# Kernel optimization log

Hardware: AMD Instinct MI355X
Metric: run time of the kernel (lower is better)

Reference implementation:

```python
import jax, jax.numpy as jnp
import numpy as np


def _conv1x1(x, W, b):
    # 1x1 conv == per-pixel channel matmul: x [B,C,H,W], W [O,C], b [O]
    return jnp.einsum('bchw,oc->bohw', x, W) + b[None, :, None, None]


def setup_inputs() -> dict:
    key = jax.random.key(0)
    ks = jax.random.split(key, 9)
    B, C, H, W = 16, 512, 32, 32
    s = 1.0 / np.sqrt(C)
    inp = {
        'x': jax.random.normal(ks[0], (B, C, H, W), dtype=jnp.float32),
        'Wq': jax.random.normal(ks[1], (C, C), dtype=jnp.float32) * s,
        'bq': jax.random.normal(ks[2], (C,), dtype=jnp.float32) * 0.01,
        'Wk': jax.random.normal(ks[3], (C, C), dtype=jnp.float32) * s,
        'bk': jax.random.normal(ks[4], (C,), dtype=jnp.float32) * 0.01,
        'Wv': jax.random.normal(ks[5], (C, C), dtype=jnp.float32) * s,
        'bv': jax.random.normal(ks[6], (C,), dtype=jnp.float32) * 0.01,
        'Wo': jax.random.normal(ks[7], (C, C), dtype=jnp.float32) * s,
        'bo': jax.random.normal(ks[8], (C,), dtype=jnp.float32) * 0.01,
    }
    return inp


def reference(x, Wq, bq, Wk, bk, Wv, bv, Wo, bo):
    B, C, H, W = x.shape
    q = _conv1x1(x, Wq, bq)
    k = _conv1x1(x, Wk, bk)
    v = _conv1x1(x, Wv, bv)
    hw = H * W
    qf = q.reshape(B, C, hw)  # [B,C,HW]
    kf = k.reshape(B, C, hw)
    vf = v.reshape(B, C, hw)
    # scores[b,i,j] = sum_c q[b,c,i] * k[b,c,j], scaled by c^-0.5
    scores = jnp.einsum('bci,bcj->bij', qf, kf) * (C ** -0.5)
    attn = jax.nn.softmax(scores, axis=2)  # softmax over keys j
    # out[b,c,i] = sum_j v[b,c,j] * attn[b,i,j]
    out = jnp.einsum('bcj,bij->bci', vf, attn).reshape(B, C, H, W)
    out = _conv1x1(out, Wo, bo)
    return x + out
```

## Files before the change

### kernel.cpp

```cpp
#include <hip/hip_runtime.h>
#include <hip/hip_bf16.h>
#include <math.h>


typedef __bf16 bf16x8 __attribute__((ext_vector_type(8)));
typedef float  f32x4  __attribute__((ext_vector_type(4)));

__device__ __forceinline__ unsigned short f2bf(float f) {
    unsigned u = __float_as_uint(f);
    u += 0x7fff + ((u >> 16) & 1);
    return (unsigned short)(u >> 16);
}

__device__ __forceinline__ void gload_lds16(const void* g, void* l) {
    __builtin_amdgcn_global_load_lds(
        (const __attribute__((address_space(1))) void*)g,
        (__attribute__((address_space(3))) void*)l, 16, 0, 0);
}

template<bool OUT_F32, int BIAS_MODE, bool RESID, int EXPM>
__global__ __launch_bounds__(256) void gemm_bt_mfma(
    const unsigned short* __restrict__ A, const unsigned short* __restrict__ B,
    void* __restrict__ Cout, const float* __restrict__ bias,
    const float* __restrict__ resid, float* __restrict__ lsum,
    int M, int N, int K, int ldA, int ldB,
    long sA, long sB, long sC, long sR,
    int ln_nn, int ln_pb, float scale)
{
    __shared__ unsigned short Als[2][128 * 32];
    __shared__ unsigned short Bls[2][128 * 32];

    const int L   = blockIdx.x;
    const int xcd = L & 7;
    const int idx = L >> 3;
    const int bz  = xcd * 2 + (idx >> ln_pb);
    const int w   = idx & ((1 << ln_pb) - 1);
    const int m0  = (w >> ln_nn) << 7;
    const int n0  = (w & ((1 << ln_nn) - 1)) << 7;

    A += bz * sA;
    B += bz * sB;

    const int tid  = threadIdx.x;
    const int lane = tid & 63;
    const int wave = tid >> 6;
    const int wm   = wave >> 1;
    const int wn   = wave & 1;

    const int ar = lane >> 2;
    const int ak = (lane & 3) * 8;

    const unsigned short* agp = A + (long)(m0 + wave * 16 + ar) * ldA + ak;
    const unsigned short* bgp = B + (long)(n0 + wave * 16 + ar) * ldB + ak;
    const long aj = 64L * ldA;
    const long bj = 64L * ldB;
    unsigned short* al0 = Als[0] + wave * 512;
    unsigned short* al0h = Als[0] + (wave + 4) * 512;
    unsigned short* al1 = Als[1] + wave * 512;
    unsigned short* al1h = Als[1] + (wave + 4) * 512;
    unsigned short* bl0 = Bls[0] + wave * 512;
    unsigned short* bl0h = Bls[0] + (wave + 4) * 512;
    unsigned short* bl1 = Bls[1] + wave * 512;
    unsigned short* bl1h = Bls[1] + (wave + 4) * 512;

    const int fr = lane & 15;
    const int fq = lane >> 4;

    f32x4 acc[4][4] = {};

    for (int k0 = 0; k0 < K; k0 += 64) {
        gload_lds16(agp,           al0);
        gload_lds16(agp + aj,      al0h);
        gload_lds16(agp + 32,      al1);
        gload_lds16(agp + 32 + aj, al1h);
        gload_lds16(bgp,           bl0);
        gload_lds16(bgp + bj,      bl0h);
        gload_lds16(bgp + 32,      bl1);
        gload_lds16(bgp + 32 + bj, bl1h);
        agp += 64; bgp += 64;
        __syncthreads();

        #pragma unroll
        for (int p = 0; p < 2; ++p) {
            bf16x8 af[4], bfr[4];
            #pragma unroll
            for (int mt = 0; mt < 4; ++mt)
                af[mt] = *(const bf16x8*)&Als[p][(wm * 64 + mt * 16 + fr) * 32 + fq * 8];
            #pragma unroll
            for (int nt = 0; nt < 4; ++nt)
                bfr[nt] = *(const bf16x8*)&Bls[p][(wn * 64 + nt * 16 + fr) * 32 + fq * 8];

            #pragma unroll
            for (int mt = 0; mt < 4; ++mt)
                #pragma unroll
                for (int nt = 0; nt < 4; ++nt)
                    acc[mt][nt] = __builtin_amdgcn_mfma_f32_16x16x32_bf16(
                        af[mt], bfr[nt], acc[mt][nt], 0, 0, 0);
        }
        __syncthreads();
    }

    float* Cf = (float*)Cout + bz * sC;
    unsigned short* Ch = (unsigned short*)Cout + bz * sC;
    if (RESID) resid += bz * sR;

    if (EXPM == 1) {
        float* lrow = lsum + bz * (long)M;
        #pragma unroll
        for (int mt = 0; mt < 4; ++mt) {
            const int row = m0 + wm * 64 + mt * 16 + fq * 4;
            #pragma unroll
            for (int r = 0; r < 4; ++r) {
                float rs = 0.0f;
                #pragma unroll
                for (int nt = 0; nt < 4; ++nt) {
                    const int col = n0 + wn * 64 + nt * 16 + fr;
                    const float e = __expf(acc[mt][nt][r] * scale);
                    rs += e;
                    Ch[(long)(row + r) * N + col] = f2bf(e);
                }
                rs += __shfl_xor(rs, 1);
                rs += __shfl_xor(rs, 2);
                rs += __shfl_xor(rs, 4);
                rs += __shfl_xor(rs, 8);
                if (fr == 0) atomicAdd(&lrow[row + r], rs);
            }
        }
    } else {
        float linv[4][4];
        if (EXPM == 2) {
            const float* lrow = lsum + bz * (long)M;
            #pragma unroll
            for (int mt = 0; mt < 4; ++mt)
                #pragma unroll
                for (int r = 0; r < 4; ++r)
                    linv[mt][r] = 1.0f / lrow[m0 + wm * 64 + mt * 16 + fq * 4 + r];
        }
        #pragma unroll
        for (int nt = 0; nt < 4; ++nt) {
            const int col = n0 + wn * 64 + nt * 16 + fr;
            const float bn = (BIAS_MODE == 2) ? bias[col] : 0.0f;
            #pragma unroll
            for (int mt = 0; mt < 4; ++mt) {
                const int row = m0 + wm * 64 + mt * 16 + fq * 4;
                #pragma unroll
                for (int r = 0; r < 4; ++r) {
                    float val = acc[mt][nt][r] + bn;
                    if (BIAS_MODE == 1) val += bias[row + r];
                    if (EXPM == 2) val *= linv[mt][r];
                    const long idx = (long)(row + r) * N + col;
                    if (RESID) val += resid[idx];
                    if (OUT_F32) Cf[idx] = val;
                    else         Ch[idx] = f2bf(val);
                }
            }
        }
    }
}

__global__ __launch_bounds__(256) void prep_all(
    const float* __restrict__ x, unsigned short* __restrict__ xT,
    const float* __restrict__ Wq, const float* __restrict__ Wk,
    const float* __restrict__ Wv, const float* __restrict__ Wo,
    const float* __restrict__ bq, const float* __restrict__ bk,
    unsigned short* __restrict__ Wb, float* __restrict__ biasqk,
    float* __restrict__ lsum)
{
    const int b = blockIdx.x;
    const int t = threadIdx.x;
    if (b < 8192) {
        __shared__ float tl[32][33];
        const int batch = b >> 9;
        const int rem = b & 511;
        const int p0 = (rem & 31) * 32;
        const int c0 = (rem >> 5) * 32;
        const float* xb = x + (long)batch * 524288;
        unsigned short* xTb = xT + (long)batch * 524288;
        const int tx = t & 31;
        const int ty = t >> 5;
        #pragma unroll
        for (int i = 0; i < 4; ++i)
            tl[ty + 8 * i][tx] = xb[(long)(c0 + ty + 8 * i) * 1024 + p0 + tx];
        __syncthreads();
        #pragma unroll
        for (int i = 0; i < 4; ++i)
            xTb[(long)(p0 + ty + 8 * i) * 512 + c0 + tx] = f2bf(tl[tx][ty + 8 * i]);
    } else if (b < 9216) {
        const int wb = b - 8192;
        const float* srcs[4] = {Wq, Wk, Wv, Wo};
        const float* s = srcs[wb >> 8];
        unsigned short* d = Wb + (long)(wb >> 8) * 262144;
        const int i = ((wb & 255) * 256 + t) * 4;
        const float4 f = *(const float4*)(s + i);
        ushort4 h;
        h.x = f2bf(f.x); h.y = f2bf(f.y); h.z = f2bf(f.z); h.w = f2bf(f.w);
        *(ushort4*)(d + i) = h;
    } else {
        biasqk[t]       = bq[t];
        biasqk[256 + t] = bq[256 + t];
        biasqk[512 + t] = bk[t];
        biasqk[768 + t] = bk[256 + t];
        #pragma unroll
        for (int i = 0; i < 64; ++i) lsum[i * 256 + t] = 0.0f;
    }
}

extern "C" void kernel_launch(void* const* d_in, const int* in_sizes, int n_in,
                              void* d_out, int out_size, void* d_ws, size_t ws_size,
                              hipStream_t stream)
{
    const float* x  = (const float*)d_in[0];
    const float* Wq = (const float*)d_in[1];
    const float* bq = (const float*)d_in[2];
    const float* Wk = (const float*)d_in[3];
    const float* bk = (const float*)d_in[4];
    const float* Wv = (const float*)d_in[5];
    const float* bv = (const float*)d_in[6];
    const float* Wo = (const float*)d_in[7];
    const float* bo = (const float*)d_in[8];
    float* out = (float*)d_out;

    const int Bn = 16, C = 512, HW = 1024;
    const long CHW = (long)C * HW;
    const long SHW = (long)HW * HW;

    unsigned short* xT   = (unsigned short*)d_ws;
    unsigned short* qkT  = xT + Bn * CHW;
    unsigned short* vB   = qkT + Bn * SHW;
    unsigned short* expS = vB + Bn * CHW;
    unsigned short* Wb   = expS + Bn * SHW;
    float* biasqk = (float*)(Wb + 4 * 262144);
    float* lsum   = biasqk + 1024;
    unsigned short* OT = xT;

    unsigned short* Wvb = Wb + 2 * 262144;
    unsigned short* Wob = Wb + 3 * 262144;

    const dim3 blk(256);
    const float scale = 0.044194173824159216f;

    prep_all<<<dim3(9217), blk, 0, stream>>>(x, xT, Wq, Wk, Wv, Wo, bq, bk,
                                             Wb, biasqk, lsum);

    gemm_bt_mfma<false, 2, false, 0><<<dim3(1024), blk, 0, stream>>>(
        xT, Wb, qkT, biasqk, nullptr, nullptr,
        HW, 2 * C, C, C, C, CHW, 0, SHW, 0, 3, 6, 0.0f);

    gemm_bt_mfma<false, 1, false, 0><<<dim3(512), blk, 0, stream>>>(
        Wvb, xT, vB, bv, nullptr, nullptr,
        C, HW, C, C, C, 0, CHW, CHW, 0, 3, 5, 0.0f);

    gemm_bt_mfma<false, 0, false, 1><<<dim3(1024), blk, 0, stream>>>(
        qkT, qkT + C, expS, nullptr, nullptr, lsum,
        HW, HW, C, 2 * C, 2 * C, SHW, SHW, SHW, 0, 3, 6, scale);

    gemm_bt_mfma<false, 0, false, 2><<<dim3(512), blk, 0, stream>>>(
        expS, vB, OT, nullptr, nullptr, lsum,
        HW, C, HW, HW, HW, SHW, CHW, CHW, 0, 2, 5, 0.0f);

    gemm_bt_mfma<true, 1, true, 0><<<dim3(512), blk, 0, stream>>>(
        Wob, OT, out, bo, x, nullptr,
        C, HW, C, C, C, 0, CHW, CHW, CHW, 3, 5, 0.0f);
}
```

Baseline: 217.6 us.

## Fold Wv into Wo and attention scale into Wq, dropping the V projection GEMM

Precomputes Wvo = Wo·Wv and bvo = Wo·bv + bo, so attention is applied directly to bf16 x and then projected once by Wvo. This folding of bv relies on softmax rows summing to 1. It removes the separate V-projection GEMM, and it pre-scales Wq and bq by C^-0.5 so the scores epilogue no longer multiplies. In exchange, prep writes an extra bf16 copy of x and runs a small weight GEMM plus a bias matvec. The residual is now read from bf16 x instead of fp32 x, which loses some accuracy.

```diff
diff --git a/kernel.cpp b/kernel.cpp
--- a/kernel.cpp
+++ b/kernel.cpp
@@ -12,31 +12,41 @@
     return (unsigned short)(u >> 16);
 }
 
+__device__ __forceinline__ float bf2f(unsigned short h) {
+    return __uint_as_float(((unsigned)h) << 16);
+}
+
 __device__ __forceinline__ void gload_lds16(const void* g, void* l) {
     __builtin_amdgcn_global_load_lds(
         (const __attribute__((address_space(1))) void*)g,
         (__attribute__((address_space(3))) void*)l, 16, 0, 0);
 }
 
-template<bool OUT_F32, int BIAS_MODE, bool RESID, int EXPM>
+template<bool OUT_F32, int BIAS_MODE, int RESID, int EXPM, int DECODE>
 __global__ __launch_bounds__(256) void gemm_bt_mfma(
     const unsigned short* __restrict__ A, const unsigned short* __restrict__ B,
     void* __restrict__ Cout, const float* __restrict__ bias,
-    const float* __restrict__ resid, float* __restrict__ lsum,
+    const unsigned short* __restrict__ resid, float* __restrict__ lsum,
     int M, int N, int K, int ldA, int ldB,
     long sA, long sB, long sC, long sR,
-    int ln_nn, int ln_pb, float scale)
+    int ln_nn, int ln_pb)
 {
     __shared__ unsigned short Als[2][128 * 32];
     __shared__ unsigned short Bls[2][128 * 32];
 
-    const int L   = blockIdx.x;
-    const int xcd = L & 7;
-    const int idx = L >> 3;
-    const int bz  = xcd * 2 + (idx >> ln_pb);
-    const int w   = idx & ((1 << ln_pb) - 1);
-    const int m0  = (w >> ln_nn) << 7;
-    const int n0  = (w & ((1 << ln_nn) - 1)) << 7;
+    const int L = blockIdx.x;
+    int bz, w;
+    if (DECODE == 1) {
+        const int xcd = L & 7;
+        const int idx = L >> 3;
+        bz = xcd * 2 + (idx >> ln_pb);
+        w  = idx & ((1 << ln_pb) - 1);
+    } else {
+        bz = 0;
+        w  = L;
+    }
+    const int m0 = (w >> ln_nn) << 7;
+    const int n0 = (w & ((1 << ln_nn) - 1)) << 7;
 
     A += bz * sA;
     B += bz * sB;
@@ -54,13 +64,13 @@
     const unsigned short* bgp = B + (long)(n0 + wave * 16 + ar) * ldB + ak;
     const long aj = 64L * ldA;
     const long bj = 64L * ldB;
-    unsigned short* al0 = Als[0] + wave * 512;
+    unsigned short* al0  = Als[0] + wave * 512;
     unsigned short* al0h = Als[0] + (wave + 4) * 512;
-    unsigned short* al1 = Als[1] + wave * 512;
+    unsigned short* al1  = Als[1] + wave * 512;
     unsigned short* al1h = Als[1] + (wave + 4) * 512;
-    unsigned short* bl0 = Bls[0] + wave * 512;
+    unsigned short* bl0  = Bls[0] + wave * 512;
     unsigned short* bl0h = Bls[0] + (wave + 4) * 512;
-    unsigned short* bl1 = Bls[1] + wave * 512;
+    unsigned short* bl1  = Bls[1] + wave * 512;
     unsigned short* bl1h = Bls[1] + (wave + 4) * 512;
 
     const int fr = lane & 15;
@@ -115,7 +125,7 @@
                 #pragma unroll
                 for (int nt = 0; nt < 4; ++nt) {
                     const int col = n0 + wn * 64 + nt * 16 + fr;
-                    const float e = __expf(acc[mt][nt][r] * scale);
+                    const float e = __expf(acc[mt][nt][r]);
                     rs += e;
                     Ch[(long)(row + r) * N + col] = f2bf(e);
                 }
@@ -149,7 +159,7 @@
                     if (BIAS_MODE == 1) val += bias[row + r];
                     if (EXPM == 2) val *= linv[mt][r];
                     const long idx = (long)(row + r) * N + col;
-                    if (RESID) val += resid[idx];
+                    if (RESID == 2) val += bf2f(resid[idx]);
                     if (OUT_F32) Cf[idx] = val;
                     else         Ch[idx] = f2bf(val);
                 }
@@ -159,15 +169,21 @@
 }
 
 __global__ __launch_bounds__(256) void prep_all(
-    const float* __restrict__ x, unsigned short* __restrict__ xT,
+    const float* __restrict__ x,
+    unsigned short* __restrict__ xT, unsigned short* __restrict__ xbf,
     const float* __restrict__ Wq, const float* __restrict__ Wk,
     const float* __restrict__ Wv, const float* __restrict__ Wo,
     const float* __restrict__ bq, const float* __restrict__ bk,
-    unsigned short* __restrict__ Wb, float* __restrict__ biasqk,
+    const float* __restrict__ bv, const float* __restrict__ bo,
+    unsigned short* __restrict__ Wqb, unsigned short* __restrict__ Wkb,
+    unsigned short* __restrict__ Wob, unsigned short* __restrict__ WvTb,
+    float* __restrict__ biasqk, float* __restrict__ bvo,
     float* __restrict__ lsum)
 {
+    const float s = 0.044194173824159216f;
     const int b = blockIdx.x;
     const int t = threadIdx.x;
+
     if (b < 8192) {
         __shared__ float tl[32][33];
         const int batch = b >> 9;
@@ -175,33 +191,75 @@
         const int p0 = (rem & 31) * 32;
         const int c0 = (rem >> 5) * 32;
         const float* xb = x + (long)batch * 524288;
-        unsigned short* xTb = xT + (long)batch * 524288;
+        unsigned short* xTb  = xT  + (long)batch * 524288;
+        unsigned short* xbfb = xbf + (long)batch * 524288;
         const int tx = t & 31;
         const int ty = t >> 5;
         #pragma unroll
-        for (int i = 0; i < 4; ++i)
-            tl[ty + 8 * i][tx] = xb[(long)(c0 + ty + 8 * i) * 1024 + p0 + tx];
+        for (int i = 0; i < 4; ++i) {
+            const float v = xb[(long)(c0 + ty + 8 * i) * 1024 + p0 + tx];
+            xbfb[(long)(c0 + ty + 8 * i) * 1024 + p0 + tx] = f2bf(v);
+            tl[ty + 8 * i][tx] = v;
+        }
         __syncthreads();
         #pragma unroll
         for (int i = 0; i < 4; ++i)
             xTb[(long)(p0 + ty + 8 * i) * 512 + c0 + tx] = f2bf(tl[tx][ty + 8 * i]);
-    } else if (b < 9216) {
-        const int wb = b - 8192;
-        const float* srcs[4] = {Wq, Wk, Wv, Wo};
-        const float* s = srcs[wb >> 8];
-        unsigned short* d = Wb + (long)(wb >> 8) * 262144;
-        const int i = ((wb & 255) * 256 + t) * 4;
-        const float4 f = *(const float4*)(s + i);
+    } else if (b < 8704) {
+        const bool isq = b < 8448;
+        const float* src = isq ? Wq : Wk;
+        unsigned short* dst = isq ? Wqb : Wkb;
+        const float m = isq ? s : 1.0f;
+        const int i = (((b - 8192) & 255) * 256 + t) * 4;
+        const float4 f = *(const float4*)(src + i);
+        ushort4 h;
+        h.x = f2bf(f.x * m); h.y = f2bf(f.y * m);
+        h.z = f2bf(f.z * m); h.w = f2bf(f.w * m);
+        *(ushort4*)(dst + i) = h;
+    } else if (b < 8960) {
+        const int i = ((b - 8704) * 256 + t) * 4;
+        const float4 f = *(const float4*)(Wo + i);
         ushort4 h;
         h.x = f2bf(f.x); h.y = f2bf(f.y); h.z = f2bf(f.z); h.w = f2bf(f.w);
-        *(ushort4*)(d + i) = h;
-    } else {
-        biasqk[t]       = bq[t];
-        biasqk[256 + t] = bq[256 + t];
+        *(ushort4*)(Wob + i) = h;
+    } else if (b < 9216) {
+        __shared__ float tl[32][33];
+        const int wb = b - 8960;
+        const int r0 = (wb >> 4) * 32;
+        const int c0 = (wb & 15) * 32;
+        const int tx = t & 31;
+        const int ty = t >> 5;
+        #pragma unroll
+        for (int i = 0; i < 4; ++i)
+            tl[ty + 8 * i][tx] = Wv[(long)(r0 + ty + 8 * i) * 512 + c0 + tx];
+        __syncthreads();
+        #pragma unroll
+        for (int i = 0; i < 4; ++i)
+            WvTb[(long)(c0 + ty + 8 * i) * 512 + r0 + tx] = f2bf(tl[tx][ty + 8 * i]);
+    } else if (b == 9216) {
+        biasqk[t]       = bq[t] * s;
+        biasqk[256 + t] = bq[256 + t] * s;
         biasqk[512 + t] = bk[t];
         biasqk[768 + t] = bk[256 + t];
         #pragma unroll
         for (int i = 0; i < 64; ++i) lsum[i * 256 + t] = 0.0f;
+    } else {
+        __shared__ float bvs[512];
+        bvs[t] = bv[t];
+        bvs[256 + t] = bv[256 + t];
+        __syncthreads();
+        const int lane = t & 63;
+        const int wave = t >> 6;
+        for (int o = wave; o < 512; o += 4) {
+            float p = 0.0f;
+            #pragma unroll
+            for (int c = lane; c < 512; c += 64)
+                p += Wo[(long)o * 512 + c] * bvs[c];
+            #pragma unroll
+            for (int off = 32; off > 0; off >>= 1)
+                p += __shfl_down(p, off);
+            if (lane == 0) bvo[o] = p + bo[o];
+        }
     }
 }
 
@@ -226,39 +284,41 @@
 
     unsigned short* xT   = (unsigned short*)d_ws;
     unsigned short* qkT  = xT + Bn * CHW;
-    unsigned short* vB   = qkT + Bn * SHW;
-    unsigned short* expS = vB + Bn * CHW;
-    unsigned short* Wb   = expS + Bn * SHW;
-    float* biasqk = (float*)(Wb + 4 * 262144);
-    float* lsum   = biasqk + 1024;
-    unsigned short* OT = xT;
-
-    unsigned short* Wvb = Wb + 2 * 262144;
-    unsigned short* Wob = Wb + 3 * 262144;
+    unsigned short* xbf  = qkT + Bn * SHW;
+    unsigned short* expS = xbf + Bn * CHW;
+    unsigned short* Wqb  = expS + Bn * SHW;
+    unsigned short* Wkb  = Wqb + 262144;
+    unsigned short* Wob  = Wkb + 262144;
+    unsigned short* WvTb = Wob + 262144;
+    unsigned short* Wvob = WvTb + 262144;
+    float* biasqk = (float*)(Wvob + 262144);
+    float* bvo    = biasqk + 1024;
+    float* lsum   = bvo + 512;
+    unsigned short* UT = xT;
 
     const dim3 blk(256);
-    const float scale = 0.044194173824159216f;
-
-    prep_all<<<dim3(9217), blk, 0, stream>>>(x, xT, Wq, Wk, Wv, Wo, bq, bk,
-                                             Wb, biasqk, lsum);
-
-    gemm_bt_mfma<false, 2, false, 0><<<dim3(1024), blk, 0, stream>>>(
-        xT, Wb, qkT, biasqk, nullptr, nullptr,
-        HW, 2 * C, C, C, C, CHW, 0, SHW, 0, 3, 6, 0.0f);
-
-    gemm_bt_mfma<false, 1, false, 0><<<dim3(512), blk, 0, stream>>>(
-        Wvb, xT, vB, bv, nullptr, nullptr,
-        C, HW, C, C, C, 0, CHW, CHW, 0, 3, 5, 0.0f);
-
-    gemm_bt_mfma<false, 0, false, 1><<<dim3(1024), blk, 0, stream>>>(
+
+    prep_all<<<dim3(9218), blk, 0, stream>>>(
+        x, xT, xbf, Wq, Wk, Wv, Wo, bq, bk, bv, bo,
+        Wqb, Wkb, Wob, WvTb, biasqk, bvo, lsum);
+
+    gemm_bt_mfma<false, 0, 0, 0, 0><<<dim3(16), blk, 0, stream>>>(
+        Wob, WvTb, Wvob, nullptr, nullptr, nullptr,
+        C, C, C, C, C, 0, 0, 0, 0, 2, 4);
+
+    gemm_bt_mfma<false, 2, 0, 0, 1><<<dim3(1024), blk, 0, stream>>>(
+        xT, Wqb, qkT, biasqk, nullptr, nullptr,
+        HW, 2 * C, C, C, C, CHW, 0, SHW, 0, 3, 6);
+
+    gemm_bt_mfma<false, 0, 0, 1, 1><<<dim3(1024), blk, 0, stream>>>(
         qkT, qkT + C, expS, nullptr, nullptr, lsum,
-        HW, HW, C, 2 * C, 2 * C, SHW, SHW, SHW, 0, 3, 6, scale);
-
-    gemm_bt_mfma<false, 0, false, 2><<<dim3(512), blk, 0, stream>>>(
-        expS, vB, OT, nullptr, nullptr, lsum,
-        HW, C, HW, HW, HW, SHW, CHW, CHW, 0, 2, 5, 0.0f);
-
-    gemm_bt_mfma<true, 1, true, 0><<<dim3(512), blk, 0, stream>>>(
-        Wob, OT, out, bo, x, nullptr,
-        C, HW, C, C, C, 0, CHW, CHW, CHW, 3, 5, 0.0f);
-}
+        HW, HW, C, 2 * C, 2 * C, SHW, SHW, SHW, 0, 3, 6);
+
+    gemm_bt_mfma<false, 0, 0, 2, 1><<<dim3(512), blk, 0, stream>>>(
+        expS, xbf, UT, nullptr, nullptr, lsum,
+        HW, C, HW, HW, HW, SHW, CHW, CHW, 0, 2, 5);
+
+    gemm_bt_mfma<true, 1, 2, 0, 1><<<dim3(512), blk, 0, stream>>>(
+        Wvob, UT, out, bvo, xbf, nullptr,
+        C, HW, C, C, C, 0, CHW, CHW, CHW, 3, 5);
+}
```

New measurement: 289.7 us. 33.1% more time.
